# Performance work log

Hardware: AMD Instinct MI355X
Metric: run time of the kernel (lower is better)

The kernel has to match this reference:

```python
import jax, jax.numpy as jnp
import numpy as np

# pywt db4 reconstruction filters (wavelet.rec_lo / wavelet.rec_hi)
REC_LO = np.array([0.23037781330885523, 0.7148465705525415, 0.6308807679295904,
                   -0.02798376941698385, -0.18703481171888114, 0.030841381835986965,
                   0.032883011666982945, -0.010597401784997278], dtype=np.float32)
REC_HI = np.array([-0.010597401784997278, -0.032883011666982945, 0.030841381835986965,
                   0.18703481171888114, -0.02798376941698385, -0.6308807679295904,
                   0.7148465705525415, -0.23037781330885523], dtype=np.float32)

# coefficient lengths for signal N=262144, db4 (f=8), 6 levels, mode='zero'
_LENS = {'a': 4102, 'd6': 4102, 'd5': 8198, 'd4': 16390, 'd3': 32774, 'd2': 65541, 'd1': 131075}
_B = 128


def _idwt_step(a, d, rec_lo, rec_hi):
    """One pywt idwt level (zero mode): upsample-by-2 + filter-bank synthesis.
    a, d: (B, n) -> (B, 2n - f + 2).
    Upsample (zeros between samples, len 2n-1), full convolution with the
    reconstruction filters, trim f-2 samples each side == lhs_dilation=2 with
    padding (1, 1) in a cross-correlation with flipped kernels."""
    lhs = jnp.stack([a, d], axis=1)                              # (B, 2, n)
    rhs = jnp.stack([rec_lo[::-1], rec_hi[::-1]], axis=0)[None]  # (1, 2, f) OIH
    out = jax.lax.conv_general_dilated(
        lhs, rhs, window_strides=(1,), padding=[(1, 1)],
        lhs_dilation=(2,), dimension_numbers=('NCH', 'OIH', 'NCH'))
    return out[:, 0, :]


def _waverec(a, details, rec_lo, rec_hi):
    x = a
    for d in details:  # coarsest -> finest, matching pywt.waverec
        if x.shape[-1] == d.shape[-1] + 1:  # pywt crop-by-one rule (static)
            x = x[:, :-1]
        x = _idwt_step(x, d, rec_lo, rec_hi)
    return x


def setup_inputs() -> dict:
    key = jax.random.key(0)
    keys = jax.random.split(key, len(_LENS))
    return {name: jax.random.normal(k, (_B, n), dtype=jnp.float32)
            for k, (name, n) in zip(keys, _LENS.items())}


def reference(a, d6, d5, d4, d3, d2, d1):
    rec_lo = jnp.asarray(REC_LO)
    rec_hi = jnp.asarray(REC_HI)
    return _waverec(a, (d6, d5, d4, d3, d2, d1), rec_lo, rec_hi)  # (B, 262144)
```

## Files before the change

### kernel.cpp

```cpp
#include <hip/hip_runtime.h>

#define LO0 0.23037781330885523f
#define LO1 0.7148465705525415f
#define LO2 0.6308807679295904f
#define LO3 -0.02798376941698385f
#define LO4 -0.18703481171888114f
#define LO5 0.030841381835986965f
#define LO6 0.032883011666982945f
#define LO7 -0.010597401784997278f

#define HI0 -0.010597401784997278f
#define HI1 -0.032883011666982945f
#define HI2 0.030841381835986965f
#define HI3 0.18703481171888114f
#define HI4 -0.02798376941698385f
#define HI5 -0.6308807679295904f
#define HI6 0.7148465705525415f
#define HI7 -0.23037781330885523f

#define T_OUT 4096
#define NT 256


__device__ __forceinline__ void synth_pair(
    float x0, float x1, float x2, float x3,
    float g0, float g1, float g2, float g3,
    float& e, float& o)
{
    e = x0 * LO6 + g0 * HI6;
    e = fmaf(x1, LO4, e); e = fmaf(g1, HI4, e);
    e = fmaf(x2, LO2, e); e = fmaf(g2, HI2, e);
    e = fmaf(x3, LO0, e); e = fmaf(g3, HI0, e);
    o = x0 * LO7 + g0 * HI7;
    o = fmaf(x1, LO5, o); o = fmaf(g1, HI5, o);
    o = fmaf(x2, LO3, o); o = fmaf(g2, HI3, o);
    o = fmaf(x3, LO1, o); o = fmaf(g3, HI1, o);
}

template<int NP>
__device__ __forceinline__ void level_compute(
    const float* __restrict__ XB, const float* __restrict__ D,
    float* __restrict__ OB, int tid)
{
    constexpr int NVEC = NP & ~3;
    for (int p0 = 4 * tid; p0 < NVEC; p0 += 4 * NT) {
        float4 x0 = *reinterpret_cast<const float4*>(XB + p0);
        float4 x1 = *reinterpret_cast<const float4*>(XB + p0 + 4);
        float4 g0 = *reinterpret_cast<const float4*>(D + p0);
        float4 g1 = *reinterpret_cast<const float4*>(D + p0 + 4);
        float e0,o0,e1,o1,e2,o2,e3,o3;
        synth_pair(x0.x,x0.y,x0.z,x0.w, g0.x,g0.y,g0.z,g0.w, e0,o0);
        synth_pair(x0.y,x0.z,x0.w,x1.x, g0.y,g0.z,g0.w,g1.x, e1,o1);
        synth_pair(x0.z,x0.w,x1.x,x1.y, g0.z,g0.w,g1.x,g1.y, e2,o2);
        synth_pair(x0.w,x1.x,x1.y,x1.z, g0.w,g1.x,g1.y,g1.z, e3,o3);
        *reinterpret_cast<float4*>(OB + 2*p0)     = make_float4(e0,o0,e1,o1);
        *reinterpret_cast<float4*>(OB + 2*p0 + 4) = make_float4(e2,o2,e3,o3);
    }
    if constexpr (NVEC < NP) {
        int p = NVEC + tid;
        if (p < NP) {
            float e, o;
            synth_pair(XB[p],XB[p+1],XB[p+2],XB[p+3],
                       D[p],D[p+1],D[p+2],D[p+3], e, o);
            OB[2*p]   = e;
            OB[2*p+1] = o;
        }
    }
}

__device__ __forceinline__ void synth_group4_reg(
    const float* __restrict__ XB, int p0, const float* g, float* __restrict__ OB)
{
    float4 x0 = *reinterpret_cast<const float4*>(XB + p0);
    float4 x1 = *reinterpret_cast<const float4*>(XB + p0 + 4);
    float e0,o0,e1,o1,e2,o2,e3,o3;
    synth_pair(x0.x,x0.y,x0.z,x0.w, g[0],g[1],g[2],g[3], e0,o0);
    synth_pair(x0.y,x0.z,x0.w,x1.x, g[1],g[2],g[3],g[4], e1,o1);
    synth_pair(x0.z,x0.w,x1.x,x1.y, g[2],g[3],g[4],g[5], e2,o2);
    synth_pair(x0.w,x1.x,x1.y,x1.z, g[3],g[4],g[5],g[6], e3,o3);
    *reinterpret_cast<float4*>(OB + 2*p0)     = make_float4(e0,o0,e1,o1);
    *reinterpret_cast<float4*>(OB + 2*p0 + 4) = make_float4(e2,o2,e3,o3);
}

typedef const __attribute__((address_space(1))) unsigned int* as1_u32_cptr;
typedef __attribute__((address_space(3))) unsigned int* as3_u32_ptr;

__device__ __forceinline__ void stage_async(const float* __restrict__ g,
                                            float* __restrict__ l,
                                            int n, int tid)
{
    for (int i = tid; i < n; i += NT) {
        __builtin_amdgcn_global_load_lds((as1_u32_cptr)(g + i),
                                         (as3_u32_ptr)(l + i), 4, 0, 0);
    }
}

__global__ __launch_bounds__(NT) void idwt_fused_kernel(
    const float* __restrict__ a,
    const float* __restrict__ d6, const float* __restrict__ d5,
    const float* __restrict__ d4, const float* __restrict__ d3,
    const float* __restrict__ d2, const float* __restrict__ d1,
    float* __restrict__ out)
{
    __shared__ __align__(16) float bufA[1032], bufB[2056];
    __shared__ __align__(16) float D6[72], D5[136], D4[264], D3[520], D2[1032];

    const int row = blockIdx.y;
    const int K0  = blockIdx.x * T_OUT;
    const int tid = threadIdx.x;

    const float* pa  = a  + (long long)row * 4102   + (K0 >> 6);
    const float* pd6 = d6 + (long long)row * 4102   + (K0 >> 6);
    const float* pd5 = d5 + (long long)row * 8198   + (K0 >> 5);
    const float* pd4 = d4 + (long long)row * 16390  + (K0 >> 4);
    const float* pd3 = d3 + (long long)row * 32774  + (K0 >> 3);
    const float* pd2 = d2 + (long long)row * 65541  + (K0 >> 2);
    const float* pd1 = d1 + (long long)row * 131075 + (K0 >> 1);

    stage_async(pa,  bufA, 70,   tid);
    stage_async(pd6, D6,   70,   tid);
    stage_async(pd5, D5,   134,  tid);
    stage_async(pd4, D4,   262,  tid);
    stage_async(pd3, D3,   518,  tid);
    stage_async(pd2, D2,   1029, tid);

    float d1A[7], d1B[7];
#pragma unroll
    for (int j = 0; j < 7; ++j) d1A[j] = pd1[4 * tid + j];
#pragma unroll
    for (int j = 0; j < 7; ++j) d1B[j] = pd1[4 * tid + 1024 + j];

    __syncthreads();

    level_compute<67>  (bufA, D6, bufB, tid);
    __syncthreads();
    level_compute<131> (bufB, D5, bufA, tid);
    __syncthreads();
    level_compute<259> (bufA, D4, bufB, tid);
    __syncthreads();
    level_compute<515> (bufB, D3, bufA, tid);
    __syncthreads();
    level_compute<1026>(bufA, D2, bufB, tid);
    __syncthreads();

    float* orow = out + (long long)row * 262144 + K0;
    synth_group4_reg(bufB, 4 * tid,        d1A, orow);
    synth_group4_reg(bufB, 4 * tid + 1024, d1B, orow);
}

extern "C" void kernel_launch(void* const* d_in, const int* in_sizes, int n_in,
                              void* d_out, int out_size, void* d_ws, size_t ws_size,
                              hipStream_t stream) {
    const float* a  = (const float*)d_in[0];
    const float* d6 = (const float*)d_in[1];
    const float* d5 = (const float*)d_in[2];
    const float* d4 = (const float*)d_in[3];
    const float* d3 = (const float*)d_in[4];
    const float* d2 = (const float*)d_in[5];
    const float* d1 = (const float*)d_in[6];

    float* OUT = (float*)d_out;

    dim3 block(NT);
    dim3 grid(262144 / T_OUT, 128);
    idwt_fused_kernel<<<grid, block, 0, stream>>>(a, d6, d5, d4, d3, d2, d1, OUT);
}
```

Baseline: 49.97 us.

## Split each block into independent per-wave tiles to remove block barriers

Each 64-lane wave now reconstructs its own 1024-sample output tile with private LDS buffers, so the __syncthreads between levels are removed and wave-level ordering is relied on instead. The d2 coefficients are loaded straight into registers rather than staged through LDS, and the smaller tiles shrink the LDS footprint. In exchange, the halo overlap between neighbouring tiles is recomputed per wave, so redundant loads and arithmetic go up. Correctness also depends on in-wave LDS visibility without explicit barriers.

```diff
diff --git a/kernel.cpp b/kernel.cpp
--- a/kernel.cpp
+++ b/kernel.cpp
@@ -18,7 +18,6 @@
 #define HI6 0.7148465705525415f
 #define HI7 -0.23037781330885523f
 
-#define T_OUT 4096
 #define NT 256
 
 
@@ -37,35 +36,21 @@
     o = fmaf(x3, LO1, o); o = fmaf(g3, HI1, o);
 }
 
-template<int NP>
-__device__ __forceinline__ void level_compute(
+__device__ __forceinline__ void synth_group4_lds(
     const float* __restrict__ XB, const float* __restrict__ D,
-    float* __restrict__ OB, int tid)
+    float* __restrict__ OB, int p0)
 {
-    constexpr int NVEC = NP & ~3;
-    for (int p0 = 4 * tid; p0 < NVEC; p0 += 4 * NT) {
-        float4 x0 = *reinterpret_cast<const float4*>(XB + p0);
-        float4 x1 = *reinterpret_cast<const float4*>(XB + p0 + 4);
-        float4 g0 = *reinterpret_cast<const float4*>(D + p0);
-        float4 g1 = *reinterpret_cast<const float4*>(D + p0 + 4);
-        float e0,o0,e1,o1,e2,o2,e3,o3;
-        synth_pair(x0.x,x0.y,x0.z,x0.w, g0.x,g0.y,g0.z,g0.w, e0,o0);
-        synth_pair(x0.y,x0.z,x0.w,x1.x, g0.y,g0.z,g0.w,g1.x, e1,o1);
-        synth_pair(x0.z,x0.w,x1.x,x1.y, g0.z,g0.w,g1.x,g1.y, e2,o2);
-        synth_pair(x0.w,x1.x,x1.y,x1.z, g0.w,g1.x,g1.y,g1.z, e3,o3);
-        *reinterpret_cast<float4*>(OB + 2*p0)     = make_float4(e0,o0,e1,o1);
-        *reinterpret_cast<float4*>(OB + 2*p0 + 4) = make_float4(e2,o2,e3,o3);
-    }
-    if constexpr (NVEC < NP) {
-        int p = NVEC + tid;
-        if (p < NP) {
-            float e, o;
-            synth_pair(XB[p],XB[p+1],XB[p+2],XB[p+3],
-                       D[p],D[p+1],D[p+2],D[p+3], e, o);
-            OB[2*p]   = e;
-            OB[2*p+1] = o;
-        }
-    }
+    float4 x0 = *reinterpret_cast<const float4*>(XB + p0);
+    float4 x1 = *reinterpret_cast<const float4*>(XB + p0 + 4);
+    float4 g0 = *reinterpret_cast<const float4*>(D + p0);
+    float4 g1 = *reinterpret_cast<const float4*>(D + p0 + 4);
+    float e0,o0,e1,o1,e2,o2,e3,o3;
+    synth_pair(x0.x,x0.y,x0.z,x0.w, g0.x,g0.y,g0.z,g0.w, e0,o0);
+    synth_pair(x0.y,x0.z,x0.w,x1.x, g0.y,g0.z,g0.w,g1.x, e1,o1);
+    synth_pair(x0.z,x0.w,x1.x,x1.y, g0.z,g0.w,g1.x,g1.y, e2,o2);
+    synth_pair(x0.w,x1.x,x1.y,x1.z, g0.w,g1.x,g1.y,g1.z, e3,o3);
+    *reinterpret_cast<float4*>(OB + 2*p0)     = make_float4(e0,o0,e1,o1);
+    *reinterpret_cast<float4*>(OB + 2*p0 + 4) = make_float4(e2,o2,e3,o3);
 }
 
 __device__ __forceinline__ void synth_group4_reg(
@@ -82,14 +67,34 @@
     *reinterpret_cast<float4*>(OB + 2*p0 + 4) = make_float4(e2,o2,e3,o3);
 }
 
+template<int NP>
+__device__ __forceinline__ void wave_level(
+    const float* __restrict__ XB, const float* __restrict__ D,
+    float* __restrict__ OB, int lane)
+{
+    constexpr int NVEC = NP & ~3;
+    static_assert(NVEC <= 256, "one vec group per lane");
+    if (4 * lane < NVEC) synth_group4_lds(XB, D, OB, 4 * lane);
+    if constexpr (NVEC < NP) {
+        int p = NVEC + lane;
+        if (p < NP) {
+            float e, o;
+            synth_pair(XB[p],XB[p+1],XB[p+2],XB[p+3],
+                       D[p],D[p+1],D[p+2],D[p+3], e, o);
+            OB[2*p]   = e;
+            OB[2*p+1] = o;
+        }
+    }
+}
+
 typedef const __attribute__((address_space(1))) unsigned int* as1_u32_cptr;
 typedef __attribute__((address_space(3))) unsigned int* as3_u32_ptr;
 
-__device__ __forceinline__ void stage_async(const float* __restrict__ g,
-                                            float* __restrict__ l,
-                                            int n, int tid)
+__device__ __forceinline__ void stage_async_w(const float* __restrict__ g,
+                                              float* __restrict__ l,
+                                              int n, int lane)
 {
-    for (int i = tid; i < n; i += NT) {
+    for (int i = lane; i < n; i += 64) {
         __builtin_amdgcn_global_load_lds((as1_u32_cptr)(g + i),
                                          (as3_u32_ptr)(l + i), 4, 0, 0);
     }
@@ -102,50 +107,75 @@
     const float* __restrict__ d2, const float* __restrict__ d1,
     float* __restrict__ out)
 {
-    __shared__ __align__(16) float bufA[1032], bufB[2056];
-    __shared__ __align__(16) float D6[72], D5[136], D4[264], D3[520], D2[1032];
+    __shared__ __align__(16) float sA[4][264];
+    __shared__ __align__(16) float sB[4][520];
+    __shared__ __align__(16) float sD6[4][24];
+    __shared__ __align__(16) float sD5[4][40];
+    __shared__ __align__(16) float sD4[4][72];
+    __shared__ __align__(16) float sD3[4][136];
 
-    const int row = blockIdx.y;
-    const int K0  = blockIdx.x * T_OUT;
-    const int tid = threadIdx.x;
+    const int row  = blockIdx.y;
+    const int wid  = threadIdx.x >> 6;
+    const int lane = threadIdx.x & 63;
+    const int K0w  = blockIdx.x * 4096 + wid * 1024;
 
-    const float* pa  = a  + (long long)row * 4102   + (K0 >> 6);
-    const float* pd6 = d6 + (long long)row * 4102   + (K0 >> 6);
-    const float* pd5 = d5 + (long long)row * 8198   + (K0 >> 5);
-    const float* pd4 = d4 + (long long)row * 16390  + (K0 >> 4);
-    const float* pd3 = d3 + (long long)row * 32774  + (K0 >> 3);
-    const float* pd2 = d2 + (long long)row * 65541  + (K0 >> 2);
-    const float* pd1 = d1 + (long long)row * 131075 + (K0 >> 1);
+    const float* pa  = a  + (long long)row * 4102   + (K0w >> 6);
+    const float* pd6 = d6 + (long long)row * 4102   + (K0w >> 6);
+    const float* pd5 = d5 + (long long)row * 8198   + (K0w >> 5);
+    const float* pd4 = d4 + (long long)row * 16390  + (K0w >> 4);
+    const float* pd3 = d3 + (long long)row * 32774  + (K0w >> 3);
+    const float* pd2 = d2 + (long long)row * 65541  + (K0w >> 2);
+    const float* pd1 = d1 + (long long)row * 131075 + (K0w >> 1);
 
-    stage_async(pa,  bufA, 70,   tid);
-    stage_async(pd6, D6,   70,   tid);
-    stage_async(pd5, D5,   134,  tid);
-    stage_async(pd4, D4,   262,  tid);
-    stage_async(pd3, D3,   518,  tid);
-    stage_async(pd2, D2,   1029, tid);
+    stage_async_w(pa,  sA[wid],  22,  lane);
+    stage_async_w(pd6, sD6[wid], 22,  lane);
+    stage_async_w(pd5, sD5[wid], 38,  lane);
+    stage_async_w(pd4, sD4[wid], 70,  lane);
+    stage_async_w(pd3, sD3[wid], 134, lane);
+
+    float d2r[7];
+#pragma unroll
+    for (int j = 0; j < 7; ++j) d2r[j] = pd2[4 * lane + j];
+    float d2t[4];
+    if (lane < 2) {
+#pragma unroll
+        for (int j = 0; j < 4; ++j) d2t[j] = pd2[256 + lane + j];
+    }
+
+    asm volatile("s_waitcnt vmcnt(0)" ::: "memory");
+
+    if (lane < 19) {
+        float e, o;
+        synth_pair(sA[wid][lane], sA[wid][lane+1], sA[wid][lane+2], sA[wid][lane+3],
+                   sD6[wid][lane], sD6[wid][lane+1], sD6[wid][lane+2], sD6[wid][lane+3],
+                   e, o);
+        sB[wid][2*lane]   = e;
+        sB[wid][2*lane+1] = o;
+    }
 
     float d1A[7], d1B[7];
 #pragma unroll
-    for (int j = 0; j < 7; ++j) d1A[j] = pd1[4 * tid + j];
+    for (int j = 0; j < 7; ++j) d1A[j] = pd1[4 * lane + j];
 #pragma unroll
-    for (int j = 0; j < 7; ++j) d1B[j] = pd1[4 * tid + 1024 + j];
+    for (int j = 0; j < 7; ++j) d1B[j] = pd1[4 * lane + 256 + j];
 
-    __syncthreads();
+    wave_level<35> (sB[wid], sD5[wid], sA[wid], lane);
+    wave_level<67> (sA[wid], sD4[wid], sB[wid], lane);
+    wave_level<131>(sB[wid], sD3[wid], sA[wid], lane);
 
-    level_compute<67>  (bufA, D6, bufB, tid);
-    __syncthreads();
-    level_compute<131> (bufB, D5, bufA, tid);
-    __syncthreads();
-    level_compute<259> (bufA, D4, bufB, tid);
-    __syncthreads();
-    level_compute<515> (bufB, D3, bufA, tid);
-    __syncthreads();
-    level_compute<1026>(bufA, D2, bufB, tid);
-    __syncthreads();
+    synth_group4_reg(sA[wid], 4 * lane, d2r, sB[wid]);
+    if (lane < 2) {
+        int p = 256 + lane;
+        float e, o;
+        synth_pair(sA[wid][p], sA[wid][p+1], sA[wid][p+2], sA[wid][p+3],
+                   d2t[0], d2t[1], d2t[2], d2t[3], e, o);
+        sB[wid][2*p]   = e;
+        sB[wid][2*p+1] = o;
+    }
 
-    float* orow = out + (long long)row * 262144 + K0;
-    synth_group4_reg(bufB, 4 * tid,        d1A, orow);
-    synth_group4_reg(bufB, 4 * tid + 1024, d1B, orow);
+    float* orow = out + (long long)row * 262144 + K0w;
+    synth_group4_reg(sB[wid], 4 * lane,       d1A, orow);
+    synth_group4_reg(sB[wid], 4 * lane + 256, d1B, orow);
 }
 
 extern "C" void kernel_launch(void* const* d_in, const int* in_sizes, int n_in,
@@ -162,6 +192,6 @@
     float* OUT = (float*)d_out;
 
     dim3 block(NT);
-    dim3 grid(262144 / T_OUT, 128);
+    dim3 grid(64, 128);
     idwt_fused_kernel<<<grid, block, 0, stream>>>(a, d6, d5, d4, d3, d2, d1, OUT);
 }
```

Measured after the change: 48.76 us. 2.4% less time.
